# Performance work log

Measured on AMD Instinct MI355X. Metric: run time of the kernel, lower is better.

Reference implementation:

```python
import jax, jax.numpy as jnp
import numpy as np

KH, KW = 3, 3
STRIDE, PAD, DIL = 1, 1, 1
DG = 1
B, CIN, H, W = 8, 64, 128, 128
COUT = 64


def setup_inputs() -> dict:
    key = jax.random.key(0)
    ks = jax.random.split(key, 4)
    x = jax.random.normal(ks[0], (B, CIN, H, W), jnp.float32)
    offset = jax.random.normal(ks[1], (B, 2 * DG * KH * KW, H, W), jnp.float32)
    mask = jax.random.uniform(ks[2], (B, DG * KH * KW, H, W), jnp.float32)
    stdv = 1.0 / np.sqrt(CIN * KH * KW)
    weight = jax.random.uniform(ks[3], (COUT, CIN, KH, KW), jnp.float32, -stdv, stdv)
    bias = jnp.zeros((COUT,), jnp.float32)
    return {"x": x, "offset": offset, "mask": mask, "weight": weight, "bias": bias}


def _dcn_v2(x, offset, mask, weight, bias):
    b, c, h, w = x.shape
    ho = (h + 2 * PAD - DIL * (KH - 1) - 1) // STRIDE + 1
    wo = (w + 2 * PAD - DIL * (KW - 1) - 1) // STRIDE + 1
    K = KH * KW
    cg = c // DG

    # base sampling grid per kernel tap: (K, Ho, Wo)
    base_y = (jnp.arange(ho)[None, :] * STRIDE - PAD + jnp.arange(KH)[:, None] * DIL).astype(x.dtype)
    base_x = (jnp.arange(wo)[None, :] * STRIDE - PAD + jnp.arange(KW)[:, None] * DIL).astype(x.dtype)
    grid_y = jnp.broadcast_to(base_y[:, None, :, None], (KH, KW, ho, wo)).reshape(K, ho, wo)
    grid_x = jnp.broadcast_to(base_x[None, :, None, :], (KH, KW, ho, wo)).reshape(K, ho, wo)

    # offset layout: (B, DG, K, 2[y,x], Ho, Wo)
    off = offset.reshape(b, DG, K, 2, ho, wo)
    py = grid_y + off[:, :, :, 0]  # (B, DG, K, Ho, Wo)
    px = grid_x + off[:, :, :, 1]

    y0 = jnp.floor(py)
    x0 = jnp.floor(px)
    ly, lx = py - y0, px - x0
    hy, hx = 1.0 - ly, 1.0 - lx
    y0i = y0.astype(jnp.int32)
    x0i = x0.astype(jnp.int32)

    xg = x.reshape(b, DG, cg, h * w)

    def corner(yi, xi, wgt):
        valid = ((yi >= 0) & (yi < h) & (xi >= 0) & (xi < w)).astype(x.dtype)
        idx = jnp.clip(yi, 0, h - 1) * w + jnp.clip(xi, 0, w - 1)  # (B,DG,K,Ho,Wo)
        idxf = idx.reshape(b, DG, 1, -1)
        v = jnp.take_along_axis(xg, jnp.broadcast_to(idxf, (b, DG, cg, idxf.shape[-1])), axis=-1)
        v = v.reshape(b, DG, cg, K, ho, wo)
        return v * (wgt * valid)[:, :, None]

    # bilinear sample with zero padding outside -> (B, DG, Cg, K, Ho, Wo)
    vals = (corner(y0i, x0i, hy * hx)
            + corner(y0i, x0i + 1, hy * lx)
            + corner(y0i + 1, x0i, ly * hx)
            + corner(y0i + 1, x0i + 1, ly * lx))

    # modulation mask
    vals = vals * mask.reshape(b, DG, 1, K, ho, wo)

    wk = weight.reshape(weight.shape[0], DG, cg, K)
    out = jnp.einsum('ogck,bgckhw->bohw', wk, vals) + bias[None, :, None, None]
    return out


def reference(x, offset, mask, weight, bias):
    return _dcn_v2(x, offset, mask, weight, bias)
```

## Files before the change

### kernel.cpp

```cpp
#include <hip/hip_runtime.h>

#define BATCH 8
#define CIN   64
#define COUT  64
#define Hdim  128
#define Wdim  128
#define HW    (Hdim * Wdim)

typedef unsigned short ushort_t;
typedef unsigned short ushort8 __attribute__((ext_vector_type(8)));
typedef short short8 __attribute__((ext_vector_type(8)));
typedef float f32x4 __attribute__((ext_vector_type(4)));

__device__ __forceinline__ float b2f(ushort_t u) {
    return __uint_as_float(((unsigned int)u) << 16);
}
__device__ __forceinline__ ushort_t f2b(float f) {
    unsigned int u = __float_as_uint(f);
    return (ushort_t)((u + 0x8000u) >> 16);
}

__global__ __launch_bounds__(256) void dcnv2_prep(
    const float* __restrict__ x, const float* __restrict__ w,
    ushort_t* __restrict__ xt, ushort_t* __restrict__ wt)
{
    int bid = blockIdx.x;
    if (bid < 4096) {
        int g = bid * 256 + threadIdx.x;
        int pixel = g >> 3;
        int c0 = (g & 7) << 3;
        int b = pixel >> 14, hw = pixel & (HW - 1);
        const float* xp = x + (size_t)(b * CIN + c0) * HW + hw;
        ushort8 o;
#pragma unroll
        for (int i = 0; i < 8; ++i) o[i] = f2b(xp[(size_t)i * HW]);
        *(ushort8*)(xt + (size_t)pixel * 64 + c0) = o;
    } else {
        int t2 = (bid - 4096) * 256 + threadIdx.x;
        int o = t2 >> 6, c = t2 & 63;
        const float* wp = w + (size_t)(o * 64 + c) * 9;
#pragma unroll
        for (int k = 0; k < 9; ++k) wt[k * 4096 + o * 64 + c] = f2b(wp[k]);
    }
}

__global__ __launch_bounds__(256) void dcnv2_mfma(
    const ushort_t* __restrict__ xt,
    const ushort_t* __restrict__ wt,
    const float* __restrict__ off,
    const float* __restrict__ msk,
    const float* __restrict__ bias,
    float* __restrict__ out)
{
    __shared__ ushort_t col[64 * 72];
    __shared__ ushort_t wl [64 * 72];

    int bid = blockIdx.x;
    int swz = (bid & 7) * 256 + (bid >> 3);
    int tid = threadIdx.x;
    int pbase = swz << 6;

    int p_loc = tid >> 2;
    int c0 = (tid & 3) << 4;
    int pixel = pbase + p_loc;
    int bb = pixel >> 14;
    int hw = pixel & (HW - 1);
    int y = hw >> 7, xq = hw & (Wdim - 1);

    float oy[9], ox[9], mm[9];
    const float* offb = off + (size_t)(bb * 18) * HW + hw;
    const float* mb   = msk + (size_t)(bb * 9) * HW + hw;
#pragma unroll
    for (int k = 0; k < 9; ++k) {
        oy[k] = offb[(size_t)(2 * k)     * HW];
        ox[k] = offb[(size_t)(2 * k + 1) * HW];
        mm[k] = mb  [(size_t)k * HW];
    }
    const ushort_t* xtb = xt + (size_t)bb * HW * 64;

    int lane = tid & 63;
    int wv = tid >> 6;
    int arow = wv * 16 + (lane & 15);
    int kc8 = (lane >> 4) << 3;
    f32x4 zero4 = {0.f, 0.f, 0.f, 0.f};
    f32x4 acc[4];
#pragma unroll
    for (int n = 0; n < 4; ++n) acc[n] = zero4;

#pragma unroll
    for (int k = 0; k < 9; ++k) {
        const int ky = k / 3, kx = k % 3;
        __syncthreads();

        {
            int o = tid >> 2;
            const ushort8* src = (const ushort8*)(wt + k * 4096 + o * 64 + c0);
            ushort8 w0 = src[0], w1 = src[1];
            *(ushort8*)(&wl[o * 72 + c0])     = w0;
            *(ushort8*)(&wl[o * 72 + c0 + 8]) = w1;
        }

        {
            float py = (float)(y - 1 + ky) + oy[k];
            float px = (float)(xq - 1 + kx) + ox[k];
            float fy = floorf(py), fx = floorf(px);
            float ly = py - fy, lx = px - fx;
            float hy = 1.f - ly, hx = 1.f - lx;
            int y0 = (int)fy, x0 = (int)fx;
            int y1 = y0 + 1, x1 = x0 + 1;
            float m = mm[k];
            float vy0 = (y0 >= 0 && y0 < Hdim) ? m : 0.f;
            float vy1 = (y1 >= 0 && y1 < Hdim) ? m : 0.f;
            float vx0 = (x0 >= 0 && x0 < Wdim) ? 1.f : 0.f;
            float vx1 = (x1 >= 0 && x1 < Wdim) ? 1.f : 0.f;
            float w00 = hy * hx * vy0 * vx0, w01 = hy * lx * vy0 * vx1;
            float w10 = ly * hx * vy1 * vx0, w11 = ly * lx * vy1 * vx1;
            int cy0 = min(max(y0, 0), Hdim - 1), cy1 = min(max(y1, 0), Hdim - 1);
            int cx0 = min(max(x0, 0), Wdim - 1), cx1 = min(max(x1, 0), Wdim - 1);

            const ushort_t* p00 = xtb + ((cy0 << 7) + cx0) * 64 + c0;
            const ushort_t* p01 = xtb + ((cy0 << 7) + cx1) * 64 + c0;
            const ushort_t* p10 = xtb + ((cy1 << 7) + cx0) * 64 + c0;
            const ushort_t* p11 = xtb + ((cy1 << 7) + cx1) * 64 + c0;
            ushort8 a00 = *(const ushort8*)p00, b00 = *(const ushort8*)(p00 + 8);
            ushort8 a01 = *(const ushort8*)p01, b01 = *(const ushort8*)(p01 + 8);
            ushort8 a10 = *(const ushort8*)p10, b10 = *(const ushort8*)(p10 + 8);
            ushort8 a11 = *(const ushort8*)p11, b11 = *(const ushort8*)(p11 + 8);

            ushort8 o0, o1;
#pragma unroll
            for (int j = 0; j < 8; ++j) {
                float v0 = w00 * b2f(a00[j]);
                v0 = fmaf(w01, b2f(a01[j]), v0);
                v0 = fmaf(w10, b2f(a10[j]), v0);
                v0 = fmaf(w11, b2f(a11[j]), v0);
                float v1 = w00 * b2f(b00[j]);
                v1 = fmaf(w01, b2f(b01[j]), v1);
                v1 = fmaf(w10, b2f(b10[j]), v1);
                v1 = fmaf(w11, b2f(b11[j]), v1);
                o0[j] = f2b(v0);
                o1[j] = f2b(v1);
            }
            *(ushort8*)(&col[p_loc * 72 + c0])     = o0;
            *(ushort8*)(&col[p_loc * 72 + c0 + 8]) = o1;
        }

        __syncthreads();

#pragma unroll
        for (int s = 0; s < 2; ++s) {
            short8 afrag = *(const short8*)(&col[arow * 72 + s * 32 + kc8]);
#pragma unroll
            for (int n = 0; n < 4; ++n) {
                short8 bfrag = *(const short8*)(&wl[(n * 16 + (lane & 15)) * 72 + s * 32 + kc8]);
                acc[n] = __builtin_amdgcn_mfma_f32_16x16x32_bf16(afrag, bfrag, acc[n], 0, 0, 0);
            }
        }
    }

    int hwb = pbase & (HW - 1);
    float* ob = out + ((size_t)bb << 6) * HW;
#pragma unroll
    for (int n = 0; n < 4; ++n) {
        int o = n * 16 + (lane & 15);
        float bv = bias[o];
#pragma unroll
        for (int j = 0; j < 4; ++j) {
            int ploc = wv * 16 + ((lane >> 4) << 2) + j;
            ob[((size_t)o << 14) + hwb + ploc] = acc[n][j] + bv;
        }
    }
}

__global__ __launch_bounds__(256) void dcnv2_direct(
    const float* __restrict__ x, const float* __restrict__ off,
    const float* __restrict__ msk, const float* __restrict__ wgt,
    const float* __restrict__ bias, float* __restrict__ out)
{
    int p = blockIdx.x * 256 + threadIdx.x;
    int b = p >> 14;
    int hw = p & (HW - 1);
    int y = hw >> 7;
    int xq = hw & (Wdim - 1);
    float acc[COUT];
#pragma unroll
    for (int o = 0; o < COUT; ++o) acc[o] = 0.0f;
    const float* xb = x + b * CIN * HW;
    const float* offb = off + b * 18 * HW + hw;
    const float* mb = msk + b * 9 * HW + hw;
    for (int k = 0; k < 9; ++k) {
        int ky = k / 3, kx = k % 3;
        float py = (float)(y - 1 + ky) + offb[(2 * k) * HW];
        float px = (float)(xq - 1 + kx) + offb[(2 * k + 1) * HW];
        float m = mb[k * HW];
        float fy = floorf(py), fx = floorf(px);
        float ly = py - fy, lx = px - fx;
        float hy = 1.0f - ly, hx = 1.0f - lx;
        int y0 = (int)fy, x0 = (int)fx;
        int y1 = y0 + 1, x1 = x0 + 1;
        float vy0 = (y0 >= 0 && y0 < Hdim) ? 1.f : 0.f;
        float vy1 = (y1 >= 0 && y1 < Hdim) ? 1.f : 0.f;
        float vx0 = (x0 >= 0 && x0 < Wdim) ? 1.f : 0.f;
        float vx1 = (x1 >= 0 && x1 < Wdim) ? 1.f : 0.f;
        float w00 = hy * hx * vy0 * vx0 * m, w01 = hy * lx * vy0 * vx1 * m;
        float w10 = ly * hx * vy1 * vx0 * m, w11 = ly * lx * vy1 * vx1 * m;
        int cy0 = min(max(y0, 0), Hdim - 1), cy1 = min(max(y1, 0), Hdim - 1);
        int cx0 = min(max(x0, 0), Wdim - 1), cx1 = min(max(x1, 0), Wdim - 1);
        int i00 = cy0 * Wdim + cx0, i01 = cy0 * Wdim + cx1;
        int i10 = cy1 * Wdim + cx0, i11 = cy1 * Wdim + cx1;
        const float* wk = wgt + k;
        const float* xc = xb;
        for (int c = 0; c < CIN; ++c) {
            float val = w00 * xc[i00] + w01 * xc[i01] + w10 * xc[i10] + w11 * xc[i11];
            const float* wc = wk + c * 9;
#pragma unroll
            for (int o = 0; o < COUT; ++o)
                acc[o] = fmaf(wc[o * (CIN * 9)], val, acc[o]);
            xc += HW;
        }
    }
    float* op = out + b * COUT * HW + hw;
#pragma unroll
    for (int o = 0; o < COUT; ++o) op[o * HW] = acc[o] + bias[o];
}

extern "C" void kernel_launch(void* const* d_in, const int* in_sizes, int n_in,
                              void* d_out, int out_size, void* d_ws, size_t ws_size,
                              hipStream_t stream) {
    const float* x    = (const float*)d_in[0];
    const float* off  = (const float*)d_in[1];
    const float* msk  = (const float*)d_in[2];
    const float* wgt  = (const float*)d_in[3];
    const float* bias = (const float*)d_in[4];
    float* out = (float*)d_out;

    const size_t xt_elems = (size_t)BATCH * HW * 64;
    const size_t wt_elems = 9 * 4096;
    const size_t need = (xt_elems + wt_elems) * sizeof(ushort_t);

    if (ws_size < need) {
        dcnv2_direct<<<(BATCH * HW) / 256, 256, 0, stream>>>(x, off, msk, wgt, bias, out);
        return;
    }

    ushort_t* xt = (ushort_t*)d_ws;
    ushort_t* wt = xt + xt_elems;

    dcnv2_prep<<<4096 + 16, 256, 0, stream>>>(x, wgt, xt, wt);
    dcnv2_mfma<<<2048, 256, 0, stream>>>(xt, wt, off, msk, bias, out);
}
```

Measured before the change: 58.25 us.

## Double-buffer col tile, read weights from global, swizzle LDS, packed bf16 math

```diff
diff --git a/kernel.cpp b/kernel.cpp
--- a/kernel.cpp
+++ b/kernel.cpp
@@ -10,14 +10,24 @@
 typedef unsigned short ushort_t;
 typedef unsigned short ushort8 __attribute__((ext_vector_type(8)));
 typedef short short8 __attribute__((ext_vector_type(8)));
+typedef unsigned int u32x4 __attribute__((ext_vector_type(4)));
+typedef float f32x2 __attribute__((ext_vector_type(2)));
 typedef float f32x4 __attribute__((ext_vector_type(4)));
 
-__device__ __forceinline__ float b2f(ushort_t u) {
-    return __uint_as_float(((unsigned int)u) << 16);
-}
 __device__ __forceinline__ ushort_t f2b(float f) {
     unsigned int u = __float_as_uint(f);
     return (ushort_t)((u + 0x8000u) >> 16);
+}
+__device__ __forceinline__ f32x2 unpk(unsigned int u) {
+    f32x2 v;
+    v.x = __uint_as_float(u << 16);
+    v.y = __uint_as_float(u & 0xffff0000u);
+    return v;
+}
+__device__ __forceinline__ unsigned int pack2(f32x2 v) {
+    unsigned int lo = (__float_as_uint(v.x) + 0x8000u) >> 16;
+    unsigned int hi = (__float_as_uint(v.y) + 0x8000u) & 0xffff0000u;
+    return lo | hi;
 }
 
 __global__ __launch_bounds__(256) void dcnv2_prep(
@@ -52,108 +62,101 @@
     const float* __restrict__ bias,
     float* __restrict__ out)
 {
-    __shared__ ushort_t col[64 * 72];
-    __shared__ ushort_t wl [64 * 72];
+    __shared__ ushort_t col[2][64 * 64];
 
     int bid = blockIdx.x;
     int swz = (bid & 7) * 256 + (bid >> 3);
     int tid = threadIdx.x;
     int pbase = swz << 6;
 
-    int p_loc = tid >> 2;
-    int c0 = (tid & 3) << 4;
-    int pixel = pbase + p_loc;
+    int lane = tid & 63;
+    int wv = tid >> 6;
+
+    int p  = lane;
+    int c0 = wv << 4;
+    int q  = p & 7;
+    int pixel = pbase + p;
     int bb = pixel >> 14;
     int hw = pixel & (HW - 1);
     int y = hw >> 7, xq = hw & (Wdim - 1);
 
-    float oy[9], ox[9], mm[9];
     const float* offb = off + (size_t)(bb * 18) * HW + hw;
     const float* mb   = msk + (size_t)(bb * 9) * HW + hw;
-#pragma unroll
-    for (int k = 0; k < 9; ++k) {
-        oy[k] = offb[(size_t)(2 * k)     * HW];
-        ox[k] = offb[(size_t)(2 * k + 1) * HW];
-        mm[k] = mb  [(size_t)k * HW];
-    }
-    const ushort_t* xtb = xt + (size_t)bb * HW * 64;
-
-    int lane = tid & 63;
-    int wv = tid >> 6;
-    int arow = wv * 16 + (lane & 15);
-    int kc8 = (lane >> 4) << 3;
-    f32x4 zero4 = {0.f, 0.f, 0.f, 0.f};
+    const ushort_t* xtb = xt + (((size_t)bb << 14) << 6);
+
+    int arow = (wv << 4) + (lane & 15);
+    int asw  = arow & 7;
+    int hi4  = lane >> 4;
+    const ushort_t* wtl = wt + (lane & 15) * 64 + (hi4 << 3);
+
     f32x4 acc[4];
 #pragma unroll
-    for (int n = 0; n < 4; ++n) acc[n] = zero4;
+    for (int n = 0; n < 4; ++n) acc[n] = (f32x4){0.f, 0.f, 0.f, 0.f};
 
 #pragma unroll
     for (int k = 0; k < 9; ++k) {
         const int ky = k / 3, kx = k % 3;
+
+        float oyk = offb[(size_t)(2 * k) * HW];
+        float oxk = offb[(size_t)(2 * k + 1) * HW];
+        float mk  = mb[(size_t)k * HW];
+
+        float py = (float)(y - 1 + ky) + oyk;
+        float px = (float)(xq - 1 + kx) + oxk;
+        float fy = floorf(py), fx = floorf(px);
+        float ly = py - fy, lx = px - fx;
+        float hy = 1.f - ly, hx = 1.f - lx;
+        int y0 = (int)fy, x0 = (int)fx;
+        int y1 = y0 + 1, x1 = x0 + 1;
+        float vy0 = (y0 >= 0 && y0 < Hdim) ? mk : 0.f;
+        float vy1 = (y1 >= 0 && y1 < Hdim) ? mk : 0.f;
+        float vx0 = (x0 >= 0 && x0 < Wdim) ? 1.f : 0.f;
+        float vx1 = (x1 >= 0 && x1 < Wdim) ? 1.f : 0.f;
+        float w00 = hy * hx * vy0 * vx0, w01 = hy * lx * vy0 * vx1;
+        float w10 = ly * hx * vy1 * vx0, w11 = ly * lx * vy1 * vx1;
+        int cy0 = min(max(y0, 0), Hdim - 1), cy1 = min(max(y1, 0), Hdim - 1);
+        int cx0 = min(max(x0, 0), Wdim - 1), cx1 = min(max(x1, 0), Wdim - 1);
+
+        const ushort_t* p00 = xtb + (((cy0 << 7) + cx0) << 6) + c0;
+        const ushort_t* p01 = xtb + (((cy0 << 7) + cx1) << 6) + c0;
+        const ushort_t* p10 = xtb + (((cy1 << 7) + cx0) << 6) + c0;
+        const ushort_t* p11 = xtb + (((cy1 << 7) + cx1) << 6) + c0;
+        u32x4 a00 = *(const u32x4*)p00, b00 = *(const u32x4*)(p00 + 8);
+        u32x4 a01 = *(const u32x4*)p01, b01 = *(const u32x4*)(p01 + 8);
+        u32x4 a10 = *(const u32x4*)p10, b10 = *(const u32x4*)(p10 + 8);
+        u32x4 a11 = *(const u32x4*)p11, b11 = *(const u32x4*)(p11 + 8);
+
+        u32x4 olo, ohi;
+#pragma unroll
+        for (int i = 0; i < 4; ++i) {
+            f32x2 v = unpk(a00[i]) * w00;
+            v += unpk(a01[i]) * w01;
+            v += unpk(a10[i]) * w10;
+            v += unpk(a11[i]) * w11;
+            olo[i] = pack2(v);
+            f32x2 u = unpk(b00[i]) * w00;
+            u += unpk(b01[i]) * w01;
+            u += unpk(b10[i]) * w10;
+            u += unpk(b11[i]) * w11;
+            ohi[i] = pack2(u);
+        }
+
+        ushort_t* cbw = &col[k & 1][p << 6];
+        *(u32x4*)(cbw + ((((wv << 1))     ^ q) << 3)) = olo;
+        *(u32x4*)(cbw + ((((wv << 1) | 1) ^ q) << 3)) = ohi;
+
         __syncthreads();
 
-        {
-            int o = tid >> 2;
-            const ushort8* src = (const ushort8*)(wt + k * 4096 + o * 64 + c0);
-            ushort8 w0 = src[0], w1 = src[1];
-            *(ushort8*)(&wl[o * 72 + c0])     = w0;
-            *(ushort8*)(&wl[o * 72 + c0 + 8]) = w1;
-        }
-
-        {
-            float py = (float)(y - 1 + ky) + oy[k];
-            float px = (float)(xq - 1 + kx) + ox[k];
-            float fy = floorf(py), fx = floorf(px);
-            float ly = py - fy, lx = px - fx;
-            float hy = 1.f - ly, hx = 1.f - lx;
-            int y0 = (int)fy, x0 = (int)fx;
-            int y1 = y0 + 1, x1 = x0 + 1;
-            float m = mm[k];
-            float vy0 = (y0 >= 0 && y0 < Hdim) ? m : 0.f;
-            float vy1 = (y1 >= 0 && y1 < Hdim) ? m : 0.f;
-            float vx0 = (x0 >= 0 && x0 < Wdim) ? 1.f : 0.f;
-            float vx1 = (x1 >= 0 && x1 < Wdim) ? 1.f : 0.f;
-            float w00 = hy * hx * vy0 * vx0, w01 = hy * lx * vy0 * vx1;
-            float w10 = ly * hx * vy1 * vx0, w11 = ly * lx * vy1 * vx1;
-            int cy0 = min(max(y0, 0), Hdim - 1), cy1 = min(max(y1, 0), Hdim - 1);
-            int cx0 = min(max(x0, 0), Wdim - 1), cx1 = min(max(x1, 0), Wdim - 1);
-
-            const ushort_t* p00 = xtb + ((cy0 << 7) + cx0) * 64 + c0;
-            const ushort_t* p01 = xtb + ((cy0 << 7) + cx1) * 64 + c0;
-            const ushort_t* p10 = xtb + ((cy1 << 7) + cx0) * 64 + c0;
-            const ushort_t* p11 = xtb + ((cy1 << 7) + cx1) * 64 + c0;
-            ushort8 a00 = *(const ushort8*)p00, b00 = *(const ushort8*)(p00 + 8);
-            ushort8 a01 = *(const ushort8*)p01, b01 = *(const ushort8*)(p01 + 8);
-            ushort8 a10 = *(const ushort8*)p10, b10 = *(const ushort8*)(p10 + 8);
-            ushort8 a11 = *(const ushort8*)p11, b11 = *(const ushort8*)(p11 + 8);
-
-            ushort8 o0, o1;
-#pragma unroll
-            for (int j = 0; j < 8; ++j) {
-                float v0 = w00 * b2f(a00[j]);
-                v0 = fmaf(w01, b2f(a01[j]), v0);
-                v0 = fmaf(w10, b2f(a10[j]), v0);
-                v0 = fmaf(w11, b2f(a11[j]), v0);
-                float v1 = w00 * b2f(b00[j]);
-                v1 = fmaf(w01, b2f(b01[j]), v1);
-                v1 = fmaf(w10, b2f(b10[j]), v1);
-                v1 = fmaf(w11, b2f(b11[j]), v1);
-                o0[j] = f2b(v0);
-                o1[j] = f2b(v1);
-            }
-            *(ushort8*)(&col[p_loc * 72 + c0])     = o0;
-            *(ushort8*)(&col[p_loc * 72 + c0 + 8]) = o1;
-        }
-
-        __syncthreads();
-
+        const ushort_t* cbr = &col[k & 1][0];
+        const ushort_t* wtk = wtl + k * 4096;
 #pragma unroll
         for (int s = 0; s < 2; ++s) {
-            short8 afrag = *(const short8*)(&col[arow * 72 + s * 32 + kc8]);
+            int ch = ((s << 2) + hi4) ^ asw;
+            short8 af = *(const short8*)(cbr + (arow << 6) + (ch << 3));
 #pragma unroll
             for (int n = 0; n < 4; ++n) {
-                short8 bfrag = *(const short8*)(&wl[(n * 16 + (lane & 15)) * 72 + s * 32 + kc8]);
-                acc[n] = __builtin_amdgcn_mfma_f32_16x16x32_bf16(afrag, bfrag, acc[n], 0, 0, 0);
+                short8 bf = *(const short8*)(wtk + n * 1024 + s * 32);
+                acc[n] = __builtin_amdgcn_mfma_f32_16x16x32_bf16(af, bf, acc[n], 0, 0, 0);
             }
         }
     }
@@ -166,7 +169,7 @@
         float bv = bias[o];
 #pragma unroll
         for (int j = 0; j < 4; ++j) {
-            int ploc = wv * 16 + ((lane >> 4) << 2) + j;
+            int ploc = (wv << 4) + ((lane >> 4) << 2) + j;
             ob[((size_t)o << 14) + hwb + ploc] = acc[n][j] + bv;
         }
     }
@@ -177,9 +180,9 @@
     const float* __restrict__ msk, const float* __restrict__ wgt,
     const float* __restrict__ bias, float* __restrict__ out)
 {
-    int p = blockIdx.x * 256 + threadIdx.x;
-    int b = p >> 14;
-    int hw = p & (HW - 1);
+    int pg = blockIdx.x * 256 + threadIdx.x;
+    int b = pg >> 14;
+    int hw = pg & (HW - 1);
     int y = hw >> 7;
     int xq = hw & (Wdim - 1);
     float acc[COUT];
```

Result: slower. 147.1 us (+152.6%).
